# Kernel tuning notes

Hardware: AMD Instinct MI355X
Metric: run time of the kernel (lower is better)

## Reference

```python
import jax, jax.numpy as jnp
import numpy as np

TOP_K = 2

def setup_inputs() -> dict:
    key = jax.random.key(0)
    k1, k2 = jax.random.split(key)
    hidden_states = jax.random.normal(k1, (16384, 4096), dtype=jnp.float32)
    W = jax.random.normal(k2, (64, 4096), dtype=jnp.float32) * 0.02  # classifier weight [num_experts, hidden]
    return {"hidden_states": hidden_states, "W": W}

def reference(hidden_states, W):
    # router logits: [T, E]
    router_logits = jnp.einsum('th,eh->te', hidden_states, W)
    # softmax in float32 (matches dtype=torch.float)
    router_probs = jax.nn.softmax(router_logits.astype(jnp.float32), axis=-1)
    # top-k over experts, then renormalize selected weights
    topk_weight, topk_experts_index = jax.lax.top_k(router_probs, TOP_K)
    topk_weight = topk_weight / jnp.sum(topk_weight, axis=-1, keepdims=True)
    return (topk_weight, router_logits, topk_experts_index)
```

## Files before the change

### kernel.cpp

```cpp
#include <hip/hip_runtime.h>
#include <hip/hip_bf16.h>

constexpr int T   = 16384;
constexpr int HD  = 4096;
constexpr int E   = 64;
constexpr int BK  = 64;
constexpr int NCH = HD / BK;
constexpr int BM  = 32;

using short8 = __attribute__((ext_vector_type(8))) short;
using f32x4  = __attribute__((ext_vector_type(4))) float;

#define AS1 __attribute__((address_space(1)))
#define AS3 __attribute__((address_space(3)))

__device__ __forceinline__ unsigned short f2bf(float x) {
  union { float f; unsigned u; } v; v.f = x;
  return (unsigned short)((v.u + 0x7FFFu + ((v.u >> 16) & 1u)) >> 16);
}
__device__ __forceinline__ float bf2f(unsigned short h) {
  union { float f; unsigned u; } v; v.u = ((unsigned)h) << 16;
  return v.f;
}

__device__ __forceinline__ void gload16(const void* g, void* l) {
  __builtin_amdgcn_global_load_lds((const AS1 void*)g, (AS3 void*)l, 16, 0, 0);
}

__global__ __launch_bounds__(256) void wprep(const float* __restrict__ W,
                                             short* __restrict__ img) {
  const int tid = blockIdx.x * 256 + threadIdx.x;
  const int c    = tid >> 10;
  const int e    = (tid >> 4) & 63;
  const int sp   = tid & 15;
  const int part = sp >> 3;
  const int g    = (sp & 7) ^ (e & 7);
  const float* src = W + (size_t)e * HD + c * BK + g * 8;
  short8 v;
#pragma unroll
  for (int j = 0; j < 8; ++j) {
    float x = src[j];
    unsigned short h = f2bf(x);
    v[j] = part ? (short)f2bf(x - bf2f(h)) : (short)h;
  }
  *(short8*)(img + (size_t)tid * 8) = v;
}

__global__ __launch_bounds__(512, 4) void router_gemm(
    const float* __restrict__ H, const short* __restrict__ img,
    float* __restrict__ logits, float* __restrict__ topw, float* __restrict__ topi) {
  __shared__ __align__(16) char lds[75776];
  char* const ldsA = lds;
  char* const ldsB = lds + 24576;
  float* const cand = (float*)(lds + 73728);

  const int tid  = threadIdx.x;
  const int w    = tid >> 6;
  const int lane = tid & 63;
  const int q    = lane >> 4;
  const int r    = lane & 15;
  const int rt   = w >> 2;
  const int ct   = w & 3;
  const int row0 = blockIdx.x * BM;

  f32x4 acc = {0.f, 0.f, 0.f, 0.f};

  auto stageA = [&](int c, int buf) {
    const int R  = tid >> 4;
    const int sp = tid & 15;
    const int s  = (sp & 8) | ((sp & 7) ^ (R & 7));
    const char* src = (const char*)(H + (size_t)(row0 + R) * HD + c * BK) + s * 16;
    gload16(src, ldsA + buf * 8192 + w * 1024);
  };
  auto stageB = [&](int c, int buf) {
    const char* srcb = (const char*)img + (size_t)c * 16384;
    char* dstb = ldsB + buf * 16384;
#pragma unroll
    for (int j = 0; j < 2; ++j)
      gload16(srcb + (size_t)(j * 512 + tid) * 16, dstb + (j * 512 + w * 64) * 16);
  };

  const int Arow = 16 * rt + r;
  const int ra   = r & 7;

  auto cvtpk = [&](float x, float y, unsigned& hw, unsigned& lw) {
    union { __hip_bfloat162 b; unsigned u; } Hh, Ll;
    Hh.b = __float22bfloat162_rn(float2{x, y});
    float2 hf = __bfloat1622float2(Hh.b);
    Ll.b = __float22bfloat162_rn(float2{x - hf.x, y - hf.y});
    hw = Hh.u; lw = Ll.u;
  };

  auto compute = [&](int abuf, int bbuf) {
    const char* Ab = ldsA + abuf * 8192 + Arow * 256;
    const char* Bb = ldsB + bbuf * 16384 + (16 * ct + r) * 256;
#pragma unroll
    for (int kk = 0; kk < 2; ++kk) {
      const int s0  = 8 * kk + 2 * q;
      const int sp0 = (s0 & 8) | ((s0 & 7) ^ ra);
      const int s1  = s0 + 1;
      const int sp1 = (s1 & 8) | ((s1 & 7) ^ ra);
      f32x4 a0 = *(const f32x4*)(Ab + sp0 * 16);
      f32x4 a1 = *(const f32x4*)(Ab + sp1 * 16);
      const int gh  = 4 * kk + q;
      const int sph = gh ^ ra;
      short8 bh = *(const short8*)(Bb + sph * 16);
      short8 bl = *(const short8*)(Bb + (8 | sph) * 16);
      union { short8 s; unsigned u[4]; } AH, AL;
      cvtpk(a0[0], a0[1], AH.u[0], AL.u[0]);
      cvtpk(a0[2], a0[3], AH.u[1], AL.u[1]);
      cvtpk(a1[0], a1[1], AH.u[2], AL.u[2]);
      cvtpk(a1[2], a1[3], AH.u[3], AL.u[3]);
      acc = __builtin_amdgcn_mfma_f32_16x16x32_bf16(AH.s, bh, acc, 0, 0, 0);
      acc = __builtin_amdgcn_mfma_f32_16x16x32_bf16(AL.s, bh, acc, 0, 0, 0);
      acc = __builtin_amdgcn_mfma_f32_16x16x32_bf16(AH.s, bl, acc, 0, 0, 0);
    }
  };

  stageA(0, 0);
  stageB(0, 0);
  stageA(1, 1);
  stageB(1, 1);

  int ab = 0, bb = 0;
  for (int t = 0; t < NCH - 2; ++t) {
    asm volatile("s_waitcnt vmcnt(3)\n\ts_barrier" ::: "memory");
    int nb = ab + 2; if (nb >= 3) nb -= 3;
    stageA(t + 2, nb);
    stageB(t + 2, nb);
    compute(ab, bb);
    ab = (ab == 2) ? 0 : ab + 1;
    bb = ab;
  }
  asm volatile("s_waitcnt vmcnt(3)\n\ts_barrier" ::: "memory");
  compute(ab, bb);
  ab = (ab == 2) ? 0 : ab + 1;
  bb = ab;
  asm volatile("s_waitcnt vmcnt(0)\n\ts_barrier" ::: "memory");
  compute(ab, bb);

  const int orow0 = row0 + 16 * rt + 4 * q;
#pragma unroll
  for (int rr = 0; rr < 4; ++rr)
    logits[(size_t)(orow0 + rr) * E + 16 * ct + r] = acc[rr];

#pragma unroll
  for (int rr = 0; rr < 4; ++rr) {
    const int myi = 16 * ct + r;
    float v1 = acc[rr]; int i1 = myi;
#pragma unroll
    for (int off = 1; off < 16; off <<= 1) {
      float ov = __shfl_xor(v1, off); int oi = __shfl_xor(i1, off);
      if (ov > v1 || (ov == v1 && oi < i1)) { v1 = ov; i1 = oi; }
    }
    float v2 = (myi == i1) ? -3.4e38f : acc[rr]; int i2 = myi;
#pragma unroll
    for (int off = 1; off < 16; off <<= 1) {
      float ov = __shfl_xor(v2, off); int oi = __shfl_xor(i2, off);
      if (ov > v2 || (ov == v2 && oi < i2)) { v2 = ov; i2 = oi; }
    }
    if (r == 0) {
      float* cd = cand + ((size_t)(16 * rt + 4 * q + rr) * 4 + ct) * 4;
      cd[0] = v1; cd[1] = (float)i1; cd[2] = v2; cd[3] = (float)i2;
    }
  }
  __syncthreads();

  if (tid < BM) {
    const float* cd = cand + (size_t)tid * 16;
    float bv = -3.4e38f; int bi = 1 << 30;
#pragma unroll
    for (int j = 0; j < 8; ++j) {
      float v = cd[2 * j]; int i = (int)cd[2 * j + 1];
      if (v > bv || (v == bv && i < bi)) { bv = v; bi = i; }
    }
    float sv = -3.4e38f; int si = 1 << 30;
#pragma unroll
    for (int j = 0; j < 8; ++j) {
      float v = cd[2 * j]; int i = (int)cd[2 * j + 1];
      if (i != bi && (v > sv || (v == sv && i < si))) { sv = v; si = i; }
    }
    const float w1 = 1.0f / (1.0f + __expf(sv - bv));
    const int R = row0 + tid;
    topw[(size_t)R * 2 + 0] = w1;
    topw[(size_t)R * 2 + 1] = 1.0f - w1;
    topi[(size_t)R * 2 + 0] = (float)bi;
    topi[(size_t)R * 2 + 1] = (float)si;
  }
}

extern "C" void kernel_launch(void* const* d_in, const int* in_sizes, int n_in,
                              void* d_out, int out_size, void* d_ws, size_t ws_size,
                              hipStream_t stream) {
  const float* H = (const float*)d_in[0];
  const float* W = (const float*)d_in[1];

  float* out    = (float*)d_out;
  float* topw   = out;
  float* logits = out + (size_t)T * 2;
  float* topi   = logits + (size_t)T * E;

  short* wimg = (short*)d_ws;

  wprep<<<256, 256, 0, stream>>>(W, wimg);
  router_gemm<<<T / BM, 512, 0, stream>>>(H, wimg, logits, topw, topi);
}
```

Measured before the change: 87.71 us.

## Load router weight fragments directly into registers instead of staging through LDS

The bf16 hi/lo weight image is reordered in the prep kernel so each lane can fetch its MFMA B fragments straight from global memory into double-buffered registers, removing the B tile from LDS. LDS use per block drops from about 75KB to about 26KB. That should let more blocks fit per CU and hide the streaming of the large fp32 hidden-state matrix better. The main loop is unrolled by two to alternate register buffers, with vmcnt thresholds retuned to match. In exchange it uses more VGPRs, and the weight reads now go through the cache hierarchy for every wave instead of being shared through LDS.

```diff
diff --git a/kernel.cpp b/kernel.cpp
--- a/kernel.cpp
+++ b/kernel.cpp
@@ -29,12 +29,13 @@
 
 __global__ __launch_bounds__(256) void wprep(const float* __restrict__ W,
                                              short* __restrict__ img) {
-  const int tid = blockIdx.x * 256 + threadIdx.x;
+  const int tid  = blockIdx.x * 256 + threadIdx.x;
   const int c    = tid >> 10;
-  const int e    = (tid >> 4) & 63;
-  const int sp   = tid & 15;
-  const int part = sp >> 3;
-  const int g    = (sp & 7) ^ (e & 7);
+  const int kk   = (tid >> 9) & 1;
+  const int part = (tid >> 8) & 1;
+  const int e    = (tid >> 2) & 63;
+  const int q    = tid & 3;
+  const int g    = 4 * kk + q;
   const float* src = W + (size_t)e * HD + c * BK + g * 8;
   short8 v;
 #pragma unroll
@@ -47,12 +48,11 @@
 }
 
 __global__ __launch_bounds__(512, 4) void router_gemm(
-    const float* __restrict__ H, const short* __restrict__ img,
-    float* __restrict__ logits, float* __restrict__ topw, float* __restrict__ topi) {
-  __shared__ __align__(16) char lds[75776];
+    const float* __restrict__ H, const short* img,
+    float* __restrict__ logits, float* topw, float* topi) {
+  __shared__ __align__(16) char lds[26624];
   char* const ldsA = lds;
-  char* const ldsB = lds + 24576;
-  float* const cand = (float*)(lds + 73728);
+  float* const cand = (float*)(lds + 24576);
 
   const int tid  = threadIdx.x;
   const int w    = tid >> 6;
@@ -72,12 +72,15 @@
     const char* src = (const char*)(H + (size_t)(row0 + R) * HD + c * BK) + s * 16;
     gload16(src, ldsA + buf * 8192 + w * 1024);
   };
-  auto stageB = [&](int c, int buf) {
-    const char* srcb = (const char*)img + (size_t)c * 16384;
-    char* dstb = ldsB + buf * 16384;
-#pragma unroll
-    for (int j = 0; j < 2; ++j)
-      gload16(srcb + (size_t)(j * 512 + tid) * 16, dstb + (j * 512 + w * 64) * 16);
+
+  const short* pBe = img + ((size_t)(16 * ct + r) * 4 + q) * 8;
+  short8 Bh[2][2], Bl[2][2];
+  auto loadB = [&](int t, int s) {
+#pragma unroll
+    for (int kk = 0; kk < 2; ++kk) {
+      Bh[s][kk] = *(const short8*)(pBe + (size_t)t * 8192 + kk * 4096);
+      Bl[s][kk] = *(const short8*)(pBe + (size_t)t * 8192 + kk * 4096 + 2048);
+    }
   };
 
   const int Arow = 16 * rt + r;
@@ -91,9 +94,8 @@
     hw = Hh.u; lw = Ll.u;
   };
 
-  auto compute = [&](int abuf, int bbuf) {
+  auto compute = [&](int abuf, int s) {
     const char* Ab = ldsA + abuf * 8192 + Arow * 256;
-    const char* Bb = ldsB + bbuf * 16384 + (16 * ct + r) * 256;
 #pragma unroll
     for (int kk = 0; kk < 2; ++kk) {
       const int s0  = 8 * kk + 2 * q;
@@ -102,42 +104,46 @@
       const int sp1 = (s1 & 8) | ((s1 & 7) ^ ra);
       f32x4 a0 = *(const f32x4*)(Ab + sp0 * 16);
       f32x4 a1 = *(const f32x4*)(Ab + sp1 * 16);
-      const int gh  = 4 * kk + q;
-      const int sph = gh ^ ra;
-      short8 bh = *(const short8*)(Bb + sph * 16);
-      short8 bl = *(const short8*)(Bb + (8 | sph) * 16);
-      union { short8 s; unsigned u[4]; } AH, AL;
+      union { short8 v; unsigned u[4]; } AH, AL;
       cvtpk(a0[0], a0[1], AH.u[0], AL.u[0]);
       cvtpk(a0[2], a0[3], AH.u[1], AL.u[1]);
       cvtpk(a1[0], a1[1], AH.u[2], AL.u[2]);
       cvtpk(a1[2], a1[3], AH.u[3], AL.u[3]);
-      acc = __builtin_amdgcn_mfma_f32_16x16x32_bf16(AH.s, bh, acc, 0, 0, 0);
-      acc = __builtin_amdgcn_mfma_f32_16x16x32_bf16(AL.s, bh, acc, 0, 0, 0);
-      acc = __builtin_amdgcn_mfma_f32_16x16x32_bf16(AH.s, bl, acc, 0, 0, 0);
+      acc = __builtin_amdgcn_mfma_f32_16x16x32_bf16(AH.v, Bh[s][kk], acc, 0, 0, 0);
+      acc = __builtin_amdgcn_mfma_f32_16x16x32_bf16(AL.v, Bh[s][kk], acc, 0, 0, 0);
+      acc = __builtin_amdgcn_mfma_f32_16x16x32_bf16(AH.v, Bl[s][kk], acc, 0, 0, 0);
     }
   };
 
   stageA(0, 0);
-  stageB(0, 0);
   stageA(1, 1);
-  stageB(1, 1);
-
-  int ab = 0, bb = 0;
-  for (int t = 0; t < NCH - 2; ++t) {
-    asm volatile("s_waitcnt vmcnt(3)\n\ts_barrier" ::: "memory");
-    int nb = ab + 2; if (nb >= 3) nb -= 3;
-    stageA(t + 2, nb);
-    stageB(t + 2, nb);
-    compute(ab, bb);
-    ab = (ab == 2) ? 0 : ab + 1;
-    bb = ab;
-  }
-  asm volatile("s_waitcnt vmcnt(3)\n\ts_barrier" ::: "memory");
-  compute(ab, bb);
+  loadB(0, 0);
+
+  int ab = 0;
+  for (int t = 0; t < NCH - 2; t += 2) {
+    {
+      int nb = ab + 2; if (nb >= 3) nb -= 3;
+      stageA(t + 2, nb);
+      loadB(t + 1, 1);
+      asm volatile("s_waitcnt vmcnt(5)\n\ts_barrier" ::: "memory");
+      compute(ab, 0);
+      ab = (ab == 2) ? 0 : ab + 1;
+    }
+    {
+      int nb = ab + 2; if (nb >= 3) nb -= 3;
+      stageA(t + 3, nb);
+      loadB(t + 2, 0);
+      asm volatile("s_waitcnt vmcnt(5)\n\ts_barrier" ::: "memory");
+      compute(ab, 1);
+      ab = (ab == 2) ? 0 : ab + 1;
+    }
+  }
+  loadB(NCH - 1, 1);
+  asm volatile("s_waitcnt vmcnt(5)\n\ts_barrier" ::: "memory");
+  compute(ab, 0);
   ab = (ab == 2) ? 0 : ab + 1;
-  bb = ab;
   asm volatile("s_waitcnt vmcnt(0)\n\ts_barrier" ::: "memory");
-  compute(ab, bb);
+  compute(ab, 1);
 
   const int orow0 = row0 + 16 * rt + 4 * q;
 #pragma unroll
```

Measured after the change: 97.28 us. +10.9%, slower.
